# Optimization experiments

Measured on AMD Instinct MI355X. Metric: run time of the kernel, lower is better.

Reference implementation:

```python
import jax, jax.numpy as jnp
import numpy as np

B, N, K, D = 2, 32768, 16, 64
EPS = 1e-6

def setup_inputs() -> dict:
    key = jax.random.key(0)
    k1, k2, k3, k4, k5, k6 = jax.random.split(key, 6)
    coords = jax.random.normal(k1, (B, N, 3), dtype=jnp.float32)
    features = jax.random.normal(k2, (B, D, N, 1), dtype=jnp.float32)
    idx = jax.random.randint(k3, (B, N, K), 0, N, dtype=jnp.int32)
    dist = jax.random.uniform(k4, (B, N, K), dtype=jnp.float32)
    conv_w = jax.random.normal(k5, (D, 10), dtype=jnp.float32) * 0.3  # 1x1 conv weight
    conv_b = jax.random.normal(k6, (D,), dtype=jnp.float32) * 0.01
    bn_gamma = jnp.ones((D,), dtype=jnp.float32)
    bn_beta = jnp.zeros((D,), dtype=jnp.float32)
    return {"coords": coords, "features": features, "dist": dist,
            "conv_w": conv_w, "conv_b": conv_b,
            "bn_gamma": bn_gamma, "bn_beta": bn_beta, "idx": idx}

def reference(coords, features, dist, conv_w, conv_b, bn_gamma, bn_beta, idx):
    # gather neighbor coords: (B, N, K, 3)
    neighbors = jax.vmap(lambda c, i: c[i])(coords, idx)
    center = jnp.broadcast_to(coords[:, :, None, :], (B, N, K, 3))
    # relative-position encoding: center | neighbor | center-neighbor | dist -> 10 channels
    concat = jnp.concatenate([center, neighbors, center - neighbors, dist[..., None]], axis=-1)
    # 1x1 conv == channel matmul: (B,N,K,10) @ (D,10)^T -> (B,N,K,D)
    x = jnp.einsum('bnkc,dc->bnkd', concat, conv_w) + conv_b
    # BatchNorm2d in training mode: batch stats over (B,N,K) per channel, eps=1e-6
    mean = jnp.mean(x, axis=(0, 1, 2))
    var = jnp.var(x, axis=(0, 1, 2))
    x = (x - mean) * jax.lax.rsqrt(var + EPS) * bn_gamma + bn_beta
    x = jax.nn.relu(x)
    x = jnp.transpose(x, (0, 3, 1, 2))  # (B, D, N, K)
    feat = jnp.broadcast_to(features, (B, D, N, K))
    return jnp.concatenate([x, feat], axis=1)  # (B, 2D, N, K)
```

## Files before the change

kernel.cpp:

```cpp
#include <hip/hip_runtime.h>

#define BB 2
#define NN 32768
#define KK 16
#define DD 64
#define NC 10
#define NMOM 65
#define NBLK1 256
#define BN_EPS 1e-6
#define DGRP 8
#define NCH 64
#define NCHUNKS (NN / NCH)

__host__ __device__ __forceinline__ constexpr int pair_idx(int i, int j) {
    return 10 + i * 10 - (i * (i - 1)) / 2 + (j - i);
}

__global__ __launch_bounds__(256) void k_moments(
    const float* __restrict__ coords, const float* __restrict__ dist,
    const int* __restrict__ idx, float* __restrict__ partials)
{
    const int tid = threadIdx.x;
    const int bn = blockIdx.x * 256 + tid;
    const int b = bn >> 15;

    float acc[NMOM];
#pragma unroll
    for (int v = 0; v < NMOM; ++v) acc[v] = 0.f;

    const float cx = coords[(size_t)bn * 3 + 0];
    const float cy = coords[(size_t)bn * 3 + 1];
    const float cz = coords[(size_t)bn * 3 + 2];
    const float* cb = coords + (size_t)b * NN * 3;

    for (int k = 0; k < KK; ++k) {
        const int j = idx[(size_t)bn * KK + k];
        const float nx = cb[(size_t)j * 3 + 0];
        const float ny = cb[(size_t)j * 3 + 1];
        const float nz = cb[(size_t)j * 3 + 2];
        const float dd = dist[(size_t)bn * KK + k];
        const float c[NC] = {cx, cy, cz, nx, ny, nz, cx - nx, cy - ny, cz - nz, dd};
#pragma unroll
        for (int i = 0; i < NC; ++i) acc[i] += c[i];
#pragma unroll
        for (int i = 0; i < NC; ++i)
#pragma unroll
            for (int jj = i; jj < NC; ++jj)
                acc[pair_idx(i, jj)] += c[i] * c[jj];
    }

    __shared__ float red[4 * NMOM];
    const int lane = tid & 63, wave = tid >> 6;
#pragma unroll
    for (int v = 0; v < NMOM; ++v) {
        float x = acc[v];
        x += __shfl_down(x, 32);
        x += __shfl_down(x, 16);
        x += __shfl_down(x, 8);
        x += __shfl_down(x, 4);
        x += __shfl_down(x, 2);
        x += __shfl_down(x, 1);
        if (lane == 0) red[wave * NMOM + v] = x;
    }
    __syncthreads();
    if (tid < NMOM) {
        float p = red[tid] + red[NMOM + tid] + red[2 * NMOM + tid] + red[3 * NMOM + tid];
        partials[blockIdx.x * NMOM + tid] = p;
    }
}

__global__ __launch_bounds__(320) void k_finalize(
    const float* __restrict__ partials,
    const float* __restrict__ conv_w, const float* __restrict__ conv_b,
    const float* __restrict__ gamma, const float* __restrict__ beta,
    float* __restrict__ wscaled, float* __restrict__ bias2)
{
    __shared__ double part[4][NMOM];
    __shared__ double sums[NMOM];
    const int tid = threadIdx.x;
    const int g = tid / NMOM, m = tid % NMOM;
    if (g < 4) {
        double s = 0.0;
        for (int blk = g * 64; blk < (g + 1) * 64; ++blk)
            s += (double)partials[blk * NMOM + m];
        part[g][m] = s;
    }
    __syncthreads();
    if (tid < NMOM)
        sums[tid] = part[0][tid] + part[1][tid] + part[2][tid] + part[3][tid];
    __syncthreads();
    if (tid < DD) {
        const double cnt = (double)BB * NN * KK;
        double mm[NC], w[NC];
#pragma unroll
        for (int c = 0; c < NC; ++c) {
            mm[c] = sums[c] / cnt;
            w[c] = (double)conv_w[tid * NC + c];
        }
        const double bd = (double)conv_b[tid];
        double wm = 0.0;
#pragma unroll
        for (int c = 0; c < NC; ++c) wm += w[c] * mm[c];
        const double mean = wm + bd;
        double ex2 = bd * bd + 2.0 * bd * wm;
#pragma unroll
        for (int i = 0; i < NC; ++i)
#pragma unroll
            for (int j = i; j < NC; ++j) {
                const double Mij = sums[pair_idx(i, j)] / cnt;
                ex2 += (i == j ? 1.0 : 2.0) * w[i] * w[j] * Mij;
            }
        const double var = ex2 - mean * mean;
        const double scale = (double)gamma[tid] / sqrt(var + BN_EPS);
        bias2[tid] = (float)((double)beta[tid] + (bd - mean) * scale);
#pragma unroll
        for (int c = 0; c < NC; ++c)
            wscaled[tid * NC + c] = (float)(w[c] * scale);
    }
}

__global__ __launch_bounds__(256) void k_x(
    const float* __restrict__ coords, const float* __restrict__ dist,
    const int* __restrict__ idx,
    const float* __restrict__ wscaled, const float* __restrict__ bias2,
    float* __restrict__ out)
{
    __shared__ float w_s[DD * NC];
    __shared__ float b2_s[DD];
    const int tid = threadIdx.x;
    for (int i = tid; i < DD * NC; i += 256) w_s[i] = wscaled[i];
    if (tid < DD) b2_s[tid] = bias2[tid];
    __syncthreads();

    const int nc   = blockIdx.x & (NCHUNKS - 1);
    const int b    = (blockIdx.x >> 9) & 1;
    const int dgrp = blockIdx.x >> 10;

    const int n_loc = tid >> 2;
    const int k0 = (tid & 3) << 2;
    const int n = nc * NCH + n_loc;
    const int bn = b * NN + n;

    const float* cc = coords + (size_t)bn * 3;
    const float cx = cc[0], cy = cc[1], cz = cc[2];
    const float* cb = coords + (size_t)b * NN * 3;

    const int4 j4 = *reinterpret_cast<const int4*>(idx + (size_t)bn * KK + k0);
    const float4 d4 = *reinterpret_cast<const float4*>(dist + (size_t)bn * KK + k0);
    const int js[4] = {j4.x, j4.y, j4.z, j4.w};
    const float dsv[4] = {d4.x, d4.y, d4.z, d4.w};

    float c[4][NC];
#pragma unroll
    for (int q = 0; q < 4; ++q) {
        const float* nc2 = cb + (size_t)js[q] * 3;
        const float nx = nc2[0], ny = nc2[1], nz = nc2[2];
        c[q][0] = cx; c[q][1] = cy; c[q][2] = cz;
        c[q][3] = nx; c[q][4] = ny; c[q][5] = nz;
        c[q][6] = cx - nx; c[q][7] = cy - ny; c[q][8] = cz - nz;
        c[q][9] = dsv[q];
    }

    const size_t cstride = (size_t)NN * KK;
    const size_t base = ((size_t)b * 2 * DD) * cstride + (size_t)n * KK + k0;

#pragma unroll
    for (int dd = 0; dd < DGRP; ++dd) {
        const int d = dgrp * DGRP + dd;
        const float b2 = b2_s[d];
        float r0 = b2, r1 = b2, r2 = b2, r3 = b2;
#pragma unroll
        for (int ch = 0; ch < NC; ++ch) {
            const float w = w_s[d * NC + ch];
            r0 += c[0][ch] * w;
            r1 += c[1][ch] * w;
            r2 += c[2][ch] * w;
            r3 += c[3][ch] * w;
        }
        float4 r;
        r.x = fmaxf(r0, 0.f); r.y = fmaxf(r1, 0.f);
        r.z = fmaxf(r2, 0.f); r.w = fmaxf(r3, 0.f);
        *reinterpret_cast<float4*>(out + base + (size_t)d * cstride) = r;
    }
}

__global__ __launch_bounds__(256) void k_feat(
    const float* __restrict__ features, float* __restrict__ out)
{
    const int t = blockIdx.x * 256 + threadIdx.x;
    const float f = features[t];
    const int bd = t >> 15;
    const int n = t & (NN - 1);
    const int b = bd >> 6;
    const int d = bd & (DD - 1);
    const size_t base = (((size_t)b * 2 * DD + DD + d) * NN + n) * KK;
    const float4 v{f, f, f, f};
    float4* p = reinterpret_cast<float4*>(out + base);
    p[0] = v; p[1] = v; p[2] = v; p[3] = v;
}

extern "C" void kernel_launch(void* const* d_in, const int* in_sizes, int n_in,
                              void* d_out, int out_size, void* d_ws, size_t ws_size,
                              hipStream_t stream) {
    const float* coords   = (const float*)d_in[0];
    const float* features = (const float*)d_in[1];
    const float* dist     = (const float*)d_in[2];
    const float* conv_w   = (const float*)d_in[3];
    const float* conv_b   = (const float*)d_in[4];
    const float* gamma    = (const float*)d_in[5];
    const float* beta     = (const float*)d_in[6];
    const int*   idx      = (const int*)d_in[7];
    float* out = (float*)d_out;

    float* partials = (float*)d_ws;
    float* wscaled  = partials + NBLK1 * NMOM;
    float* bias2    = wscaled + DD * NC;

    k_moments<<<NBLK1, 256, 0, stream>>>(coords, dist, idx, partials);
    k_finalize<<<1, 320, 0, stream>>>(partials, conv_w, conv_b, gamma, beta,
                                      wscaled, bias2);
    k_feat<<<(BB * DD * NN) / 256, 256, 0, stream>>>(features, out);
    k_x<<<(DD / DGRP) * BB * NCHUNKS, 256, 0, stream>>>(
        coords, dist, idx, wscaled, bias2, out);
}
```

Baseline: 614.7 us.

## Pad coords to float4 and fold conv weights into 7 effective channels

A new pre-kernel repacks coords into padded float4 so each neighbor gather is a single 16-byte load instead of three scalar loads. The finalize kernel folds the redundant center/neighbor/difference channels into 6 weights plus dist weight and bias, laid out as 8 floats per channel. The output kernel then computes a per-point center term once and does fewer FMAs per output, reading weights directly from global memory instead of staging them in LDS. This costs an extra kernel launch and workspace buffer, and reorders the float arithmetic slightly.

```diff
diff --git a/kernel.cpp b/kernel.cpp
--- a/kernel.cpp
+++ b/kernel.cpp
@@ -16,8 +16,18 @@
     return 10 + i * 10 - (i * (i - 1)) / 2 + (j - i);
 }
 
+__global__ __launch_bounds__(256) void k_coords4(
+    const float* __restrict__ coords, float4* __restrict__ coords4)
+{
+    const int t = blockIdx.x * 256 + threadIdx.x;
+    const float x = coords[(size_t)t * 3 + 0];
+    const float y = coords[(size_t)t * 3 + 1];
+    const float z = coords[(size_t)t * 3 + 2];
+    coords4[t] = float4{x, y, z, 0.f};
+}
+
 __global__ __launch_bounds__(256) void k_moments(
-    const float* __restrict__ coords, const float* __restrict__ dist,
+    const float4* __restrict__ coords4, const float* __restrict__ dist,
     const int* __restrict__ idx, float* __restrict__ partials)
 {
     const int tid = threadIdx.x;
@@ -28,18 +38,16 @@
 #pragma unroll
     for (int v = 0; v < NMOM; ++v) acc[v] = 0.f;
 
-    const float cx = coords[(size_t)bn * 3 + 0];
-    const float cy = coords[(size_t)bn * 3 + 1];
-    const float cz = coords[(size_t)bn * 3 + 2];
-    const float* cb = coords + (size_t)b * NN * 3;
+    const float4 cen = coords4[bn];
+    const float cx = cen.x, cy = cen.y, cz = cen.z;
+    const float4* cb4 = coords4 + (size_t)b * NN;
 
     for (int k = 0; k < KK; ++k) {
         const int j = idx[(size_t)bn * KK + k];
-        const float nx = cb[(size_t)j * 3 + 0];
-        const float ny = cb[(size_t)j * 3 + 1];
-        const float nz = cb[(size_t)j * 3 + 2];
+        const float4 nb = cb4[j];
         const float dd = dist[(size_t)bn * KK + k];
-        const float c[NC] = {cx, cy, cz, nx, ny, nz, cx - nx, cy - ny, cz - nz, dd};
+        const float c[NC] = {cx, cy, cz, nb.x, nb.y, nb.z,
+                             cx - nb.x, cy - nb.y, cz - nb.z, dd};
 #pragma unroll
         for (int i = 0; i < NC; ++i) acc[i] += c[i];
 #pragma unroll
@@ -73,7 +81,7 @@
     const float* __restrict__ partials,
     const float* __restrict__ conv_w, const float* __restrict__ conv_b,
     const float* __restrict__ gamma, const float* __restrict__ beta,
-    float* __restrict__ wscaled, float* __restrict__ bias2)
+    float* __restrict__ wfold)
 {
     __shared__ double part[4][NMOM];
     __shared__ double sums[NMOM];
@@ -112,54 +120,46 @@
             }
         const double var = ex2 - mean * mean;
         const double scale = (double)gamma[tid] / sqrt(var + BN_EPS);
-        bias2[tid] = (float)((double)beta[tid] + (bd - mean) * scale);
-#pragma unroll
-        for (int c = 0; c < NC; ++c)
-            wscaled[tid * NC + c] = (float)(w[c] * scale);
+        const double b2 = (double)beta[tid] + (bd - mean) * scale;
+        double ws[NC];
+#pragma unroll
+        for (int c = 0; c < NC; ++c) ws[c] = w[c] * scale;
+        float* wf = wfold + tid * 8;
+        wf[0] = (float)(ws[0] + ws[6]);
+        wf[1] = (float)(ws[1] + ws[7]);
+        wf[2] = (float)(ws[2] + ws[8]);
+        wf[3] = (float)(ws[3] - ws[6]);
+        wf[4] = (float)(ws[4] - ws[7]);
+        wf[5] = (float)(ws[5] - ws[8]);
+        wf[6] = (float)ws[9];
+        wf[7] = (float)b2;
     }
 }
 
 __global__ __launch_bounds__(256) void k_x(
-    const float* __restrict__ coords, const float* __restrict__ dist,
-    const int* __restrict__ idx,
-    const float* __restrict__ wscaled, const float* __restrict__ bias2,
+    const float4* __restrict__ coords4, const float* __restrict__ dist,
+    const int* __restrict__ idx, const float* __restrict__ wfold,
     float* __restrict__ out)
 {
-    __shared__ float w_s[DD * NC];
-    __shared__ float b2_s[DD];
-    const int tid = threadIdx.x;
-    for (int i = tid; i < DD * NC; i += 256) w_s[i] = wscaled[i];
-    if (tid < DD) b2_s[tid] = bias2[tid];
-    __syncthreads();
-
     const int nc   = blockIdx.x & (NCHUNKS - 1);
     const int b    = (blockIdx.x >> 9) & 1;
     const int dgrp = blockIdx.x >> 10;
+    const int tid  = threadIdx.x;
 
     const int n_loc = tid >> 2;
     const int k0 = (tid & 3) << 2;
     const int n = nc * NCH + n_loc;
     const int bn = b * NN + n;
 
-    const float* cc = coords + (size_t)bn * 3;
-    const float cx = cc[0], cy = cc[1], cz = cc[2];
-    const float* cb = coords + (size_t)b * NN * 3;
+    const float4 cen = coords4[bn];
+    const float4* cb4 = coords4 + (size_t)b * NN;
 
     const int4 j4 = *reinterpret_cast<const int4*>(idx + (size_t)bn * KK + k0);
     const float4 d4 = *reinterpret_cast<const float4*>(dist + (size_t)bn * KK + k0);
-    const int js[4] = {j4.x, j4.y, j4.z, j4.w};
-    const float dsv[4] = {d4.x, d4.y, d4.z, d4.w};
-
-    float c[4][NC];
-#pragma unroll
-    for (int q = 0; q < 4; ++q) {
-        const float* nc2 = cb + (size_t)js[q] * 3;
-        const float nx = nc2[0], ny = nc2[1], nz = nc2[2];
-        c[q][0] = cx; c[q][1] = cy; c[q][2] = cz;
-        c[q][3] = nx; c[q][4] = ny; c[q][5] = nz;
-        c[q][6] = cx - nx; c[q][7] = cy - ny; c[q][8] = cz - nz;
-        c[q][9] = dsv[q];
-    }
+    const float4 nb0 = cb4[j4.x];
+    const float4 nb1 = cb4[j4.y];
+    const float4 nb2 = cb4[j4.z];
+    const float4 nb3 = cb4[j4.w];
 
     const size_t cstride = (size_t)NN * KK;
     const size_t base = ((size_t)b * 2 * DD) * cstride + (size_t)n * KK + k0;
@@ -167,19 +167,14 @@
 #pragma unroll
     for (int dd = 0; dd < DGRP; ++dd) {
         const int d = dgrp * DGRP + dd;
-        const float b2 = b2_s[d];
-        float r0 = b2, r1 = b2, r2 = b2, r3 = b2;
-#pragma unroll
-        for (int ch = 0; ch < NC; ++ch) {
-            const float w = w_s[d * NC + ch];
-            r0 += c[0][ch] * w;
-            r1 += c[1][ch] * w;
-            r2 += c[2][ch] * w;
-            r3 += c[3][ch] * w;
-        }
+        const float4 f0 = *reinterpret_cast<const float4*>(wfold + d * 8);
+        const float4 f1 = *reinterpret_cast<const float4*>(wfold + d * 8 + 4);
+        const float s_cen = f1.w + f0.x * cen.x + f0.y * cen.y + f0.z * cen.z;
         float4 r;
-        r.x = fmaxf(r0, 0.f); r.y = fmaxf(r1, 0.f);
-        r.z = fmaxf(r2, 0.f); r.w = fmaxf(r3, 0.f);
+        r.x = fmaxf(s_cen + f0.w * nb0.x + f1.x * nb0.y + f1.y * nb0.z + f1.z * d4.x, 0.f);
+        r.y = fmaxf(s_cen + f0.w * nb1.x + f1.x * nb1.y + f1.y * nb1.z + f1.z * d4.y, 0.f);
+        r.z = fmaxf(s_cen + f0.w * nb2.x + f1.x * nb2.y + f1.y * nb2.z + f1.z * d4.z, 0.f);
+        r.w = fmaxf(s_cen + f0.w * nb3.x + f1.x * nb3.y + f1.y * nb3.z + f1.z * d4.w, 0.f);
         *reinterpret_cast<float4*>(out + base + (size_t)d * cstride) = r;
     }
 }
@@ -212,14 +207,15 @@
     const int*   idx      = (const int*)d_in[7];
     float* out = (float*)d_out;
 
-    float* partials = (float*)d_ws;
-    float* wscaled  = partials + NBLK1 * NMOM;
-    float* bias2    = wscaled + DD * NC;
-
-    k_moments<<<NBLK1, 256, 0, stream>>>(coords, dist, idx, partials);
+    float*  partials = (float*)d_ws;
+    float*  wfold    = (float*)d_ws + 24576;
+    float4* coords4  = (float4*)((float*)d_ws + 65536);
+
+    k_coords4<<<BB * NN / 256, 256, 0, stream>>>(coords, coords4);
+    k_moments<<<NBLK1, 256, 0, stream>>>(coords4, dist, idx, partials);
     k_finalize<<<1, 320, 0, stream>>>(partials, conv_w, conv_b, gamma, beta,
-                                      wscaled, bias2);
+                                      wfold);
     k_feat<<<(BB * DD * NN) / 256, 256, 0, stream>>>(features, out);
     k_x<<<(DD / DGRP) * BB * NCHUNKS, 256, 0, stream>>>(
-        coords, dist, idx, wscaled, bias2, out);
-}
+        coords4, dist, idx, wfold, out);
+}
```

Result: no change. 614.9 us (+0.0%).
